# Kernel optimization log

Hardware: AMD Instinct MI355X
Metric: run time of the kernel (lower is better)

## Reference

```python
import jax, jax.numpy as jnp
import numpy as np

N = 1024
X_DIM = 128
Y_DIM = 128
HID = 256


def setup_inputs() -> dict:
    key = jax.random.key(0)
    ks = jax.random.split(key, 8)
    x_samples = jax.random.normal(ks[0], (N, X_DIM), dtype=jnp.float32)
    y_samples = jax.random.normal(ks[1], (N, Y_DIM), dtype=jnp.float32)
    # F_func: Linear(x_dim+y_dim -> hidden), ReLU, Linear(hidden -> 1)
    W1 = jax.random.normal(ks[2], (HID, X_DIM + Y_DIM), dtype=jnp.float32) * 0.05
    b1 = jax.random.normal(ks[3], (HID,), dtype=jnp.float32) * 0.05
    w2 = jax.random.normal(ks[4], (HID,), dtype=jnp.float32) * 0.05  # Linear(hidden,1) weight
    b2 = jax.random.normal(ks[5], (), dtype=jnp.float32) * 0.05
    # baseline: Linear(y_dim -> 1)
    wb = jax.random.normal(ks[6], (Y_DIM,), dtype=jnp.float32) * 0.05
    bb = jax.random.normal(ks[7], (), dtype=jnp.float32) * 0.05
    return {"x_samples": x_samples, "y_samples": y_samples,
            "W1": W1, "b1": b1, "w2": w2, "b2": b2, "wb": wb, "bb": bb}


def reference(x_samples, y_samples, W1, b1, w2, b2, wb, bb):
    n = y_samples.shape[0]
    # Split first linear: F(x,y) first layer = x @ Wx^T + y @ Wy^T + b1
    # (identical math to Linear on concat([x, y]))
    Wx = W1[:, :X_DIM]  # [H, x_dim]
    Wy = W1[:, X_DIM:]  # [H, y_dim]
    px = x_samples @ Wx.T  # [N, H]
    py = y_samples @ Wy.T  # [N, H]

    # T0: F on paired samples (x_i, y_i) -> [N]
    T0 = jax.nn.relu(px + py + b1) @ w2 + b2

    # T1[i, j] = F(x_j, y_i): x tiled over dim 0, y tiled over dim 1
    h = jax.nn.relu(px[None, :, :] + py[:, None, :] + b1)  # [N, N, H]
    T1 = h @ w2 + b2  # [N, N]

    # baseline log-scores on y -> [N]
    log_scores = y_samples @ wb + bb

    # (T1 - log_scores) broadcasts log_scores along dim 1 (the j/x axis),
    # matching torch's [N,N,1] - [N,1] broadcast; logsumexp over dim 1.
    lse = jax.scipy.special.logsumexp(T1 - log_scores[None, :], axis=1)  # [N]
    log_n = jnp.log(jnp.asarray(n, dtype=T1.dtype))
    lower_bound = (1.0 + T0.mean() - log_scores.mean()
                   - jnp.exp(lse - log_n).mean())
    return lower_bound
```

## Files before the change

### kernel.cpp

```cpp
#include <hip/hip_runtime.h>
#include <hip/hip_fp16.h>

#define NN 1024
#define HID 256
#define XD 128

typedef _Float16 h2 __attribute__((ext_vector_type(2)));

#define WSF_BYTE_OFF 1049600
#define F_C    0
#define F_PART 1024
#define F_T0P  3072
#define F_LSP  3328

__device__ __forceinline__ h2 relu2(h2 x) {
  h2 z = {(_Float16)0, (_Float16)0};
  return __builtin_elementwise_max(x, z);
}

__device__ __forceinline__ float dot2f(h2 a, h2 b, float c) {
#if __has_builtin(__builtin_amdgcn_fdot2)
  return __builtin_amdgcn_fdot2(a, b, c, false);
#else
  return fmaf((float)a.x, (float)b.x, fmaf((float)a.y, (float)b.y, c));
#endif
}

__global__ __launch_bounds__(256) void prep_kernel(
    const float* __restrict__ x, const float* __restrict__ y,
    const float* __restrict__ W1, const float* __restrict__ b1,
    const float* __restrict__ w2, const float* __restrict__ b2p,
    const float* __restrict__ wb, const float* __restrict__ bbp,
    _Float16* __restrict__ wsh, float* __restrict__ wsf)
{
  __shared__ float sx[4][128];
  __shared__ float sy[4][128];
  __shared__ float st0[4][4];
  __shared__ float sls[4];
  const int t = threadIdx.x;
  const int blk = blockIdx.x;
  const int r0 = blk * 4;

  {
    const int rl = (t & 127) >> 5, f = t & 31;
    if (t < 128) {
      *(float4*)&sx[rl][f * 4] = *(const float4*)(x + (r0 + rl) * XD + f * 4);
    } else {
      *(float4*)&sy[rl][f * 4] = *(const float4*)(y + (r0 + rl) * XD + f * 4);
    }
  }
  __syncthreads();

  const int k = t;
  float apx[4] = {0,0,0,0};
  float apy[4] = {0,0,0,0};
  const float* wrow = W1 + k * 256;
  for (int dq = 0; dq < 32; ++dq) {
    float4 wx = *(const float4*)(wrow + dq * 4);
    float4 wy = *(const float4*)(wrow + 128 + dq * 4);
#pragma unroll
    for (int r = 0; r < 4; ++r) {
      float4 xv = *(const float4*)&sx[r][dq * 4];
      float4 yv = *(const float4*)&sy[r][dq * 4];
      apx[r] = fmaf(xv.x, wx.x, apx[r]);
      apx[r] = fmaf(xv.y, wx.y, apx[r]);
      apx[r] = fmaf(xv.z, wx.z, apx[r]);
      apx[r] = fmaf(xv.w, wx.w, apx[r]);
      apy[r] = fmaf(yv.x, wy.x, apy[r]);
      apy[r] = fmaf(yv.y, wy.y, apy[r]);
      apy[r] = fmaf(yv.z, wy.z, apy[r]);
      apy[r] = fmaf(yv.w, wy.w, apy[r]);
    }
  }
  const float b1k = b1[k];
#pragma unroll
  for (int r = 0; r < 4; ++r) apy[r] += b1k;

  {
    const int ko = k >> 3, kl = k & 7;
    _Float16* pxh = wsh;
    _Float16* pyh = wsh + 262144;
#pragma unroll
    for (int r = 0; r < 4; ++r) {
      const int j = r0 + r;
      const int idx = (j >> 6) * 16384 + ko * 512 + (j & 63) * 8 + kl;
      pxh[idx] = (_Float16)apx[r];
      pyh[idx] = (_Float16)apy[r];
    }
  }

  const float w2k = w2[k];
  const float b2v = b2p[0];
  const int wv = t >> 6, lane = t & 63;
#pragma unroll
  for (int r = 0; r < 4; ++r) {
    float v = fmaxf(apx[r] + apy[r], 0.f) * w2k;
    for (int o = 32; o > 0; o >>= 1) v += __shfl_down(v, o);
    if (lane == 0) st0[wv][r] = v;
  }

  if (t < 128) {
    const int rl = t >> 5, f = t & 31;
    float p = 0.f;
#pragma unroll
    for (int l = 0; l < 4; ++l) p = fmaf(sy[rl][f * 4 + l], wb[f * 4 + l], p);
    for (int m = 16; m > 0; m >>= 1) p += __shfl_xor(p, m);
    if (f == 0) {
      const float lsv = p + bbp[0];
      sls[rl] = lsv;
      wsf[F_C + r0 + rl] = __expf(b2v - lsv);
    }
  }
  __syncthreads();
  if (t == 0) {
    float t0s = 0.f, lss = 0.f;
#pragma unroll
    for (int r = 0; r < 4; ++r) {
      t0s += st0[0][r] + st0[1][r] + st0[2][r] + st0[3][r] + b2v;
      lss += sls[r];
    }
    wsf[F_T0P + blk] = t0s;
    wsf[F_LSP + blk] = lss;
  }
  if (blk == 0 && t < 128) {
    h2* w2h = (h2*)(wsh + 524288);
    h2 w; w.x = (_Float16)w2[2 * t]; w.y = (_Float16)w2[2 * t + 1];
    w2h[t] = w;
  }
}

__global__ __launch_bounds__(512) void main_kernel(
    const _Float16* __restrict__ wsh, float* __restrict__ wsf)
{
  __shared__ _Float16 spx[16384];
  __shared__ _Float16 spy[16384];
  const int t = threadIdx.x;
  const int tx = t & 15;
  const int ty = t >> 4;
  const int blk = blockIdx.x;
  const int bi = blk >> 4, bj = blk & 15;

  const float4* gx = (const float4*)(wsh + bj * 16384);
  const float4* gy = (const float4*)(wsh + 262144 + bi * 16384);
  const float4* gw = (const float4*)(wsh + 524288);
  float4* lx = (float4*)spx;
  float4* ly = (float4*)spy;
#pragma unroll
  for (int it = 0; it < 4; ++it) {
    lx[it * 512 + t] = gx[it * 512 + t];
    ly[it * 512 + t] = gy[it * 512 + t];
  }
  __syncthreads();

  float acc[2][4] = {{0.f,0.f,0.f,0.f},{0.f,0.f,0.f,0.f}};
  const float4* spx4 = (const float4*)spx;
  const float4* spy4 = (const float4*)spy;

#pragma unroll 2
  for (int ko = 0; ko < 32; ++ko) {
    float4 wv = gw[ko];
    float4 Af[4], Bf[2];
#pragma unroll
    for (int u = 0; u < 4; ++u) Af[u] = spx4[ko * 64 + u * 16 + tx];
#pragma unroll
    for (int v = 0; v < 2; ++v) Bf[v] = spy4[ko * 64 + v * 32 + ty];
    const h2* wq = (const h2*)&wv;
#pragma unroll
    for (int v = 0; v < 2; ++v) {
      const h2* bh = (const h2*)&Bf[v];
#pragma unroll
      for (int u = 0; u < 4; ++u) {
        const h2* ah = (const h2*)&Af[u];
        float s = acc[v][u];
#pragma unroll
        for (int p = 0; p < 4; ++p) {
          h2 uu = ah[p] + bh[p];
          uu = relu2(uu);
          s = dot2f(uu, wq[p], s);
        }
        acc[v][u] = s;
      }
    }
  }

  const float* cj = wsf + F_C + bj * 64;
  const float c0 = cj[tx], c1 = cj[16 + tx], c2 = cj[32 + tx], c3 = cj[48 + tx];
  float ts = 0.f;
#pragma unroll
  for (int v = 0; v < 2; ++v) {
    ts += __expf(acc[v][0]) * c0;
    ts += __expf(acc[v][1]) * c1;
    ts += __expf(acc[v][2]) * c2;
    ts += __expf(acc[v][3]) * c3;
  }
  for (int o = 32; o > 0; o >>= 1) ts += __shfl_down(ts, o);
  if ((t & 63) == 0) wsf[F_PART + blk * 8 + (t >> 6)] = ts;
}

__global__ __launch_bounds__(256) void fin_kernel(
    const float* __restrict__ wsf, float* __restrict__ out)
{
  __shared__ float sr[4][3];
  const int t = threadIdx.x;
  float e = 0.f;
#pragma unroll
  for (int q = 0; q < 8; ++q) e += wsf[F_PART + t + 256 * q];
  float t0 = wsf[F_T0P + t];
  float ls = wsf[F_LSP + t];
  for (int o = 32; o > 0; o >>= 1) {
    e  += __shfl_down(e, o);
    t0 += __shfl_down(t0, o);
    ls += __shfl_down(ls, o);
  }
  if ((t & 63) == 0) {
    sr[t >> 6][0] = e;
    sr[t >> 6][1] = t0;
    sr[t >> 6][2] = ls;
  }
  __syncthreads();
  if (t == 0) {
    const float es  = sr[0][0] + sr[1][0] + sr[2][0] + sr[3][0];
    const float t0s = sr[0][1] + sr[1][1] + sr[2][1] + sr[3][1];
    const float lss = sr[0][2] + sr[1][2] + sr[2][2] + sr[3][2];
    out[0] = 1.0f + t0s * (1.0f / 1024.0f) - lss * (1.0f / 1024.0f)
                  - es * (1.0f / 1048576.0f);
  }
}

extern "C" void kernel_launch(void* const* d_in, const int* in_sizes, int n_in,
                              void* d_out, int out_size, void* d_ws, size_t ws_size,
                              hipStream_t stream) {
  const float* x  = (const float*)d_in[0];
  const float* y  = (const float*)d_in[1];
  const float* W1 = (const float*)d_in[2];
  const float* b1 = (const float*)d_in[3];
  const float* w2 = (const float*)d_in[4];
  const float* b2 = (const float*)d_in[5];
  const float* wb = (const float*)d_in[6];
  const float* bb = (const float*)d_in[7];
  _Float16* wsh = (_Float16*)d_ws;
  float* wsf = (float*)((char*)d_ws + WSF_BYTE_OFF);
  float* out = (float*)d_out;

  hipLaunchKernelGGL(prep_kernel, dim3(256), dim3(256), 0, stream,
                     x, y, W1, b1, w2, b2, wb, bb, wsh, wsf);
  hipLaunchKernelGGL(main_kernel, dim3(256), dim3(512), 0, stream, wsh, wsf);
  hipLaunchKernelGGL(fin_kernel, dim3(1), dim3(256), 0, stream, wsf, out);
}
```

Baseline: 33.88 us.

## Retile pairwise MLP kernel with per-lane j and register-broadcast i blocks

The main kernel is restructured so each lane owns one x-row (j) and accumulates 16 y-rows (i) in registers. The hidden dimension is split across wave pairs, and the partial sums are combined through shared memory before the exp and reduction. The py operands are no longer staged in LDS; they are read from global memory in a new blocked layout as uniform broadcast loads, which cuts LDS traffic and raises arithmetic per loaded element. The prep kernel now uses 512 threads so the x and y projections run on separate halves, and the final kernel reads the partials as float4. The risk is higher register pressure and latency from the global loads in the inner loop.

```diff
diff --git a/kernel.cpp b/kernel.cpp
--- a/kernel.cpp
+++ b/kernel.cpp
@@ -6,6 +6,7 @@
 #define XD 128
 
 typedef _Float16 h2 __attribute__((ext_vector_type(2)));
+typedef _Float16 h4 __attribute__((ext_vector_type(4)));
 
 #define WSF_BYTE_OFF 1049600
 #define F_C    0
@@ -19,14 +20,10 @@
 }
 
 __device__ __forceinline__ float dot2f(h2 a, h2 b, float c) {
-#if __has_builtin(__builtin_amdgcn_fdot2)
   return __builtin_amdgcn_fdot2(a, b, c, false);
-#else
-  return fmaf((float)a.x, (float)b.x, fmaf((float)a.y, (float)b.y, c));
-#endif
-}
-
-__global__ __launch_bounds__(256) void prep_kernel(
+}
+
+__global__ __launch_bounds__(512) void prep_kernel(
     const float* __restrict__ x, const float* __restrict__ y,
     const float* __restrict__ W1, const float* __restrict__ b1,
     const float* __restrict__ w2, const float* __restrict__ b2p,
@@ -35,72 +32,71 @@
 {
   __shared__ float sx[4][128];
   __shared__ float sy[4][128];
+  __shared__ float spy2[4][256];
   __shared__ float st0[4][4];
   __shared__ float sls[4];
   const int t = threadIdx.x;
   const int blk = blockIdx.x;
   const int r0 = blk * 4;
 
-  {
-    const int rl = (t & 127) >> 5, f = t & 31;
-    if (t < 128) {
-      *(float4*)&sx[rl][f * 4] = *(const float4*)(x + (r0 + rl) * XD + f * 4);
-    } else {
-      *(float4*)&sy[rl][f * 4] = *(const float4*)(y + (r0 + rl) * XD + f * 4);
-    }
-  }
-  __syncthreads();
-
-  const int k = t;
-  float apx[4] = {0,0,0,0};
-  float apy[4] = {0,0,0,0};
-  const float* wrow = W1 + k * 256;
-  for (int dq = 0; dq < 32; ++dq) {
-    float4 wx = *(const float4*)(wrow + dq * 4);
-    float4 wy = *(const float4*)(wrow + 128 + dq * 4);
-#pragma unroll
-    for (int r = 0; r < 4; ++r) {
-      float4 xv = *(const float4*)&sx[r][dq * 4];
-      float4 yv = *(const float4*)&sy[r][dq * 4];
-      apx[r] = fmaf(xv.x, wx.x, apx[r]);
-      apx[r] = fmaf(xv.y, wx.y, apx[r]);
-      apx[r] = fmaf(xv.z, wx.z, apx[r]);
-      apx[r] = fmaf(xv.w, wx.w, apx[r]);
-      apy[r] = fmaf(yv.x, wy.x, apy[r]);
-      apy[r] = fmaf(yv.y, wy.y, apy[r]);
-      apy[r] = fmaf(yv.z, wy.z, apy[r]);
-      apy[r] = fmaf(yv.w, wy.w, apy[r]);
-    }
-  }
-  const float b1k = b1[k];
-#pragma unroll
-  for (int r = 0; r < 4; ++r) apy[r] += b1k;
-
-  {
-    const int ko = k >> 3, kl = k & 7;
-    _Float16* pxh = wsh;
-    _Float16* pyh = wsh + 262144;
-#pragma unroll
-    for (int r = 0; r < 4; ++r) {
-      const int j = r0 + r;
-      const int idx = (j >> 6) * 16384 + ko * 512 + (j & 63) * 8 + kl;
-      pxh[idx] = (_Float16)apx[r];
-      pyh[idx] = (_Float16)apy[r];
-    }
-  }
-
-  const float w2k = w2[k];
-  const float b2v = b2p[0];
-  const int wv = t >> 6, lane = t & 63;
-#pragma unroll
-  for (int r = 0; r < 4; ++r) {
-    float v = fmaxf(apx[r] + apy[r], 0.f) * w2k;
-    for (int o = 32; o > 0; o >>= 1) v += __shfl_down(v, o);
-    if (lane == 0) st0[wv][r] = v;
-  }
-
   if (t < 128) {
     const int rl = t >> 5, f = t & 31;
+    *(float4*)&sx[rl][f * 4] = *(const float4*)(x + (r0 + rl) * XD + f * 4);
+  } else if (t < 256) {
+    const int t2 = t - 128, rl = t2 >> 5, f = t2 & 31;
+    *(float4*)&sy[rl][f * 4] = *(const float4*)(y + (r0 + rl) * XD + f * 4);
+  }
+  __syncthreads();
+
+  const int side = t >> 8;
+  const int k = t & 255;
+  float ap[4] = {0.f, 0.f, 0.f, 0.f};
+  const float* wrow = W1 + k * 256 + side * 128;
+  const float (*sm)[128] = side ? sy : sx;
+#pragma unroll 8
+  for (int dq = 0; dq < 32; ++dq) {
+    float4 wv = *(const float4*)(wrow + dq * 4);
+#pragma unroll
+    for (int r = 0; r < 4; ++r) {
+      float4 sv = *(const float4*)&sm[r][dq * 4];
+      ap[r] = fmaf(sv.x, wv.x, ap[r]);
+      ap[r] = fmaf(sv.y, wv.y, ap[r]);
+      ap[r] = fmaf(sv.z, wv.z, ap[r]);
+      ap[r] = fmaf(sv.w, wv.w, ap[r]);
+    }
+  }
+
+  if (side == 1) {
+    const float b1k = b1[k];
+    _Float16* pyB = wsh + 262144;
+#pragma unroll
+    for (int r = 0; r < 4; ++r) {
+      ap[r] += b1k;
+      spy2[r][k] = ap[r];
+      const int i = r0 + r;
+      pyB[(((i >> 4) * 64 + (k >> 2)) * 16 + (i & 15)) * 4 + (k & 3)] = (_Float16)ap[r];
+    }
+  } else {
+#pragma unroll
+    for (int r = 0; r < 4; ++r) {
+      const int j = r0 + r;
+      wsh[((j >> 6) * 32 + (k >> 3)) * 512 + (j & 63) * 8 + (k & 7)] = (_Float16)ap[r];
+    }
+  }
+  __syncthreads();
+
+  if (side == 0) {
+    const float w2k = w2[k];
+    const int wv = t >> 6, lane = t & 63;
+#pragma unroll
+    for (int r = 0; r < 4; ++r) {
+      float v = fmaxf(ap[r] + spy2[r][k], 0.f) * w2k;
+      for (int o = 32; o > 0; o >>= 1) v += __shfl_down(v, o);
+      if (lane == 0) st0[wv][r] = v;
+    }
+  } else if ((t & 255) < 128) {
+    const int t2 = t & 255;
+    const int rl = t2 >> 5, f = t2 & 31;
     float p = 0.f;
 #pragma unroll
     for (int l = 0; l < 4; ++l) p = fmaf(sy[rl][f * 4 + l], wb[f * 4 + l], p);
@@ -108,11 +104,13 @@
     if (f == 0) {
       const float lsv = p + bbp[0];
       sls[rl] = lsv;
-      wsf[F_C + r0 + rl] = __expf(b2v - lsv);
-    }
-  }
-  __syncthreads();
+      wsf[F_C + r0 + rl] = __expf(b2p[0] - lsv);
+    }
+  }
+  __syncthreads();
+
   if (t == 0) {
+    const float b2v = b2p[0];
     float t0s = 0.f, lss = 0.f;
 #pragma unroll
     for (int r = 0; r < 4; ++r) {
@@ -123,78 +121,78 @@
     wsf[F_LSP + blk] = lss;
   }
   if (blk == 0 && t < 128) {
-    h2* w2h = (h2*)(wsh + 524288);
-    h2 w; w.x = (_Float16)w2[2 * t]; w.y = (_Float16)w2[2 * t + 1];
-    w2h[t] = w;
-  }
-}
-
-__global__ __launch_bounds__(512) void main_kernel(
+    h2 wv2;
+    wv2.x = (_Float16)w2[2 * t];
+    wv2.y = (_Float16)w2[2 * t + 1];
+    ((h2*)(wsh + 524288))[t] = wv2;
+  }
+}
+
+__global__ __launch_bounds__(256) void main_kernel(
     const _Float16* __restrict__ wsh, float* __restrict__ wsf)
 {
   __shared__ _Float16 spx[16384];
-  __shared__ _Float16 spy[16384];
+  __shared__ _Float16 sw2[256];
+  __shared__ float sComb[2][16][64];
   const int t = threadIdx.x;
-  const int tx = t & 15;
-  const int ty = t >> 4;
+  const int lane = t & 63;
+  const int w = __builtin_amdgcn_readfirstlane(t >> 6);
   const int blk = blockIdx.x;
   const int bi = blk >> 4, bj = blk & 15;
 
-  const float4* gx = (const float4*)(wsh + bj * 16384);
-  const float4* gy = (const float4*)(wsh + 262144 + bi * 16384);
-  const float4* gw = (const float4*)(wsh + 524288);
-  float4* lx = (float4*)spx;
-  float4* ly = (float4*)spy;
-#pragma unroll
-  for (int it = 0; it < 4; ++it) {
-    lx[it * 512 + t] = gx[it * 512 + t];
-    ly[it * 512 + t] = gy[it * 512 + t];
-  }
-  __syncthreads();
-
-  float acc[2][4] = {{0.f,0.f,0.f,0.f},{0.f,0.f,0.f,0.f}};
-  const float4* spx4 = (const float4*)spx;
-  const float4* spy4 = (const float4*)spy;
-
-#pragma unroll 2
-  for (int ko = 0; ko < 32; ++ko) {
-    float4 wv = gw[ko];
-    float4 Af[4], Bf[2];
-#pragma unroll
-    for (int u = 0; u < 4; ++u) Af[u] = spx4[ko * 64 + u * 16 + tx];
-#pragma unroll
-    for (int v = 0; v < 2; ++v) Bf[v] = spy4[ko * 64 + v * 32 + ty];
-    const h2* wq = (const h2*)&wv;
-#pragma unroll
-    for (int v = 0; v < 2; ++v) {
-      const h2* bh = (const h2*)&Bf[v];
-#pragma unroll
-      for (int u = 0; u < 4; ++u) {
-        const h2* ah = (const h2*)&Af[u];
-        float s = acc[v][u];
-#pragma unroll
-        for (int p = 0; p < 4; ++p) {
-          h2 uu = ah[p] + bh[p];
-          uu = relu2(uu);
-          s = dot2f(uu, wq[p], s);
-        }
-        acc[v][u] = s;
-      }
-    }
-  }
-
-  const float* cj = wsf + F_C + bj * 64;
-  const float c0 = cj[tx], c1 = cj[16 + tx], c2 = cj[32 + tx], c3 = cj[48 + tx];
-  float ts = 0.f;
-#pragma unroll
-  for (int v = 0; v < 2; ++v) {
-    ts += __expf(acc[v][0]) * c0;
-    ts += __expf(acc[v][1]) * c1;
-    ts += __expf(acc[v][2]) * c2;
-    ts += __expf(acc[v][3]) * c3;
-  }
-  for (int o = 32; o > 0; o >>= 1) ts += __shfl_down(ts, o);
-  if ((t & 63) == 0) wsf[F_PART + blk * 8 + (t >> 6)] = ts;
+  {
+    const float4* gx = (const float4*)(wsh + (size_t)bj * 16384);
+    float4* lx = (float4*)spx;
+#pragma unroll
+    for (int it = 0; it < 8; ++it) lx[it * 256 + t] = gx[it * 256 + t];
+    if (t < 32) ((float4*)sw2)[t] = ((const float4*)(wsh + 524288))[t];
+  }
+  __syncthreads();
+
+  const int isub = w & 1, khalf = w >> 1;
+  const int iblk = bi * 2 + isub;
+  const uint4* __restrict__ bB =
+      (const uint4*)(wsh + 262144) + (size_t)iblk * 512 + (size_t)khalf * 256;
+
+  float acc[16] = {0.f,0.f,0.f,0.f,0.f,0.f,0.f,0.f,
+                   0.f,0.f,0.f,0.f,0.f,0.f,0.f,0.f};
+
+#pragma unroll 4
+  for (int q = 0; q < 32; ++q) {
+    const int kq = khalf * 32 + q;
+    h4 a4 = *(const h4*)(spx + (kq >> 1) * 512 + lane * 8 + (kq & 1) * 4);
+    const h2* ap = (const h2*)&a4;
+    h4 w4 = *(const h4*)(sw2 + kq * 4);
+    const h2* wp = (const h2*)&w4;
+    uint4 b[8];
+#pragma unroll
+    for (int r = 0; r < 8; ++r) b[r] = bB[q * 8 + r];
+    const h2* bh = (const h2*)b;
+#pragma unroll
+    for (int a = 0; a < 16; ++a) {
+      float s = acc[a];
+      h2 u0 = relu2(ap[0] + bh[a * 2 + 0]);
+      s = dot2f(u0, wp[0], s);
+      h2 u1 = relu2(ap[1] + bh[a * 2 + 1]);
+      s = dot2f(u1, wp[1], s);
+      acc[a] = s;
+    }
+  }
+
+  if (w >= 2) {
+#pragma unroll
+    for (int a = 0; a < 16; ++a) sComb[isub][a][lane] = acc[a];
+  }
+  __syncthreads();
+  if (w < 2) {
+    const float cj = wsf[F_C + bj * 64 + lane];
+    float ts = 0.f;
+#pragma unroll
+    for (int a = 0; a < 16; ++a) ts += __expf(acc[a] + sComb[isub][a][lane]);
+    ts *= cj;
+    for (int o = 32; o > 0; o >>= 1) ts += __shfl_down(ts, o);
+    if (lane == 0) wsf[F_PART + blk * 2 + w] = ts;
+  }
 }
 
 __global__ __launch_bounds__(256) void fin_kernel(
@@ -202,9 +200,8 @@
 {
   __shared__ float sr[4][3];
   const int t = threadIdx.x;
-  float e = 0.f;
-#pragma unroll
-  for (int q = 0; q < 8; ++q) e += wsf[F_PART + t + 256 * q];
+  float4 ev = *(const float4*)(wsf + F_PART + t * 4);
+  float e = ev.x + ev.y + ev.z + ev.w;
   float t0 = wsf[F_T0P + t];
   float ls = wsf[F_LSP + t];
   for (int o = 32; o > 0; o >>= 1) {
@@ -242,8 +239,8 @@
   float* wsf = (float*)((char*)d_ws + WSF_BYTE_OFF);
   float* out = (float*)d_out;
 
-  hipLaunchKernelGGL(prep_kernel, dim3(256), dim3(256), 0, stream,
+  hipLaunchKernelGGL(prep_kernel, dim3(256), dim3(512), 0, stream,
                      x, y, W1, b1, w2, b2, wb, bb, wsh, wsf);
-  hipLaunchKernelGGL(main_kernel, dim3(256), dim3(512), 0, stream, wsh, wsf);
+  hipLaunchKernelGGL(main_kernel, dim3(512), dim3(256), 0, stream, wsh, wsf);
   hipLaunchKernelGGL(fin_kernel, dim3(1), dim3(256), 0, stream, wsf, out);
 }
```

Measured after the change: 40.00 us. 18.1% more time.

## Keep px rows in registers and split hidden dim across waves

Applied to the files above, without the earlier changes.

Restructures the pairwise main kernel. Each lane now holds one x-row's half of the hidden vector in registers, and waves loop over 8 y-rows read from LDS (broadcast reads). The hidden dimension is split into two halves across wave groups and combined through shared memory. The grid doubles to 512 blocks of 32 y-rows each, and prep writes a plain row-major layout. This cuts LDS traffic and the footprint per block to raise occupancy, at the cost of high register pressure (16 h8 per lane) and an extra sync and combine step.

```diff
diff --git a/kernel.cpp b/kernel.cpp
--- a/kernel.cpp
+++ b/kernel.cpp
@@ -6,6 +6,7 @@
 #define XD 128
 
 typedef _Float16 h2 __attribute__((ext_vector_type(2)));
+typedef _Float16 h8 __attribute__((ext_vector_type(8)));
 
 #define WSF_BYTE_OFF 1049600
 #define F_C    0
@@ -19,11 +20,7 @@
 }
 
 __device__ __forceinline__ float dot2f(h2 a, h2 b, float c) {
-#if __has_builtin(__builtin_amdgcn_fdot2)
   return __builtin_amdgcn_fdot2(a, b, c, false);
-#else
-  return fmaf((float)a.x, (float)b.x, fmaf((float)a.y, (float)b.y, c));
-#endif
 }
 
 __global__ __launch_bounds__(256) void prep_kernel(
@@ -77,15 +74,13 @@
   for (int r = 0; r < 4; ++r) apy[r] += b1k;
 
   {
-    const int ko = k >> 3, kl = k & 7;
     _Float16* pxh = wsh;
     _Float16* pyh = wsh + 262144;
 #pragma unroll
     for (int r = 0; r < 4; ++r) {
       const int j = r0 + r;
-      const int idx = (j >> 6) * 16384 + ko * 512 + (j & 63) * 8 + kl;
-      pxh[idx] = (_Float16)apx[r];
-      pyh[idx] = (_Float16)apy[r];
+      pxh[j * 256 + k] = (_Float16)apx[r];
+      pyh[j * 256 + k] = (_Float16)apy[r];
     }
   }
 
@@ -123,78 +118,86 @@
     wsf[F_LSP + blk] = lss;
   }
   if (blk == 0 && t < 128) {
-    h2* w2h = (h2*)(wsh + 524288);
-    h2 w; w.x = (_Float16)w2[2 * t]; w.y = (_Float16)w2[2 * t + 1];
-    w2h[t] = w;
-  }
-}
-
-__global__ __launch_bounds__(512) void main_kernel(
+    h2 wv2;
+    wv2.x = (_Float16)w2[2 * t];
+    wv2.y = (_Float16)w2[2 * t + 1];
+    ((h2*)(wsh + 524288))[t] = wv2;
+  }
+}
+
+__global__ __launch_bounds__(512, 4) void main_kernel(
     const _Float16* __restrict__ wsh, float* __restrict__ wsf)
 {
-  __shared__ _Float16 spx[16384];
-  __shared__ _Float16 spy[16384];
+  __shared__ _Float16 spy[32 * 256];
+  __shared__ _Float16 sw2[256];
+  __shared__ float sComb[4][8][64];
   const int t = threadIdx.x;
-  const int tx = t & 15;
-  const int ty = t >> 4;
+  const int lane = t & 63;
+  const int w = t >> 6;
   const int blk = blockIdx.x;
-  const int bi = blk >> 4, bj = blk & 15;
-
-  const float4* gx = (const float4*)(wsh + bj * 16384);
-  const float4* gy = (const float4*)(wsh + 262144 + bi * 16384);
-  const float4* gw = (const float4*)(wsh + 524288);
-  float4* lx = (float4*)spx;
-  float4* ly = (float4*)spy;
-#pragma unroll
-  for (int it = 0; it < 4; ++it) {
-    lx[it * 512 + t] = gx[it * 512 + t];
-    ly[it * 512 + t] = gy[it * 512 + t];
-  }
-  __syncthreads();
-
-  float acc[2][4] = {{0.f,0.f,0.f,0.f},{0.f,0.f,0.f,0.f}};
-  const float4* spx4 = (const float4*)spx;
-  const float4* spy4 = (const float4*)spy;
-
+  const int bj = blk & 15;
+  const int i0 = (blk >> 4) * 32;
+  const int khalf = w >> 2;
+  const int iset = w & 3;
+
+  h8 pxr[16];
+  {
+    const float4* gpx = (const float4*)(wsh + (size_t)(bj * 64 + lane) * 256
+                                            + khalf * 128);
+#pragma unroll
+    for (int it = 0; it < 16; ++it) ((float4*)pxr)[it] = gpx[it];
+  }
+  {
+    const float4* gpy = (const float4*)(wsh + 262144 + (size_t)i0 * 256);
+    float4* lpy = (float4*)spy;
+    lpy[t] = gpy[t];
+    lpy[t + 512] = gpy[t + 512];
+    if (t < 32) ((float4*)sw2)[t] = ((const float4*)(wsh + 524288))[t];
+  }
+  __syncthreads();
+
+  const float cj = wsf[F_C + bj * 64 + lane];
+
+  const _Float16* w2k = sw2 + khalf * 128;
+  float sacc[8];
 #pragma unroll 2
-  for (int ko = 0; ko < 32; ++ko) {
-    float4 wv = gw[ko];
-    float4 Af[4], Bf[2];
-#pragma unroll
-    for (int u = 0; u < 4; ++u) Af[u] = spx4[ko * 64 + u * 16 + tx];
-#pragma unroll
-    for (int v = 0; v < 2; ++v) Bf[v] = spy4[ko * 64 + v * 32 + ty];
-    const h2* wq = (const h2*)&wv;
-#pragma unroll
-    for (int v = 0; v < 2; ++v) {
-      const h2* bh = (const h2*)&Bf[v];
+  for (int ii = 0; ii < 8; ++ii) {
+    const _Float16* prow = spy + (iset * 8 + ii) * 256 + khalf * 128;
+    float s0 = 0.f, s1 = 0.f, s2 = 0.f, s3 = 0.f;
+#pragma unroll
+    for (int q = 0; q < 16; q += 4) {
 #pragma unroll
       for (int u = 0; u < 4; ++u) {
-        const h2* ah = (const h2*)&Af[u];
-        float s = acc[v][u];
-#pragma unroll
-        for (int p = 0; p < 4; ++p) {
-          h2 uu = ah[p] + bh[p];
-          uu = relu2(uu);
-          s = dot2f(uu, wq[p], s);
-        }
-        acc[v][u] = s;
+        h8 pv = *(const h8*)(prow + (q + u) * 8);
+        h8 wv = *(const h8*)(w2k + (q + u) * 8);
+        const h2* p2 = (const h2*)&pv;
+        const h2* w2p = (const h2*)&wv;
+        const h2* x2 = (const h2*)&pxr[q + u];
+        float s = (u == 0) ? s0 : (u == 1) ? s1 : (u == 2) ? s2 : s3;
+        s = dot2f(relu2(x2[0] + p2[0]), w2p[0], s);
+        s = dot2f(relu2(x2[1] + p2[1]), w2p[1], s);
+        s = dot2f(relu2(x2[2] + p2[2]), w2p[2], s);
+        s = dot2f(relu2(x2[3] + p2[3]), w2p[3], s);
+        if (u == 0) s0 = s; else if (u == 1) s1 = s; else if (u == 2) s2 = s; else s3 = s;
       }
     }
-  }
-
-  const float* cj = wsf + F_C + bj * 64;
-  const float c0 = cj[tx], c1 = cj[16 + tx], c2 = cj[32 + tx], c3 = cj[48 + tx];
-  float ts = 0.f;
-#pragma unroll
-  for (int v = 0; v < 2; ++v) {
-    ts += __expf(acc[v][0]) * c0;
-    ts += __expf(acc[v][1]) * c1;
-    ts += __expf(acc[v][2]) * c2;
-    ts += __expf(acc[v][3]) * c3;
-  }
-  for (int o = 32; o > 0; o >>= 1) ts += __shfl_down(ts, o);
-  if ((t & 63) == 0) wsf[F_PART + blk * 8 + (t >> 6)] = ts;
+    sacc[ii] = (s0 + s1) + (s2 + s3);
+  }
+
+  if (khalf == 1) {
+#pragma unroll
+    for (int ii = 0; ii < 8; ++ii) sComb[iset][ii][lane] = sacc[ii];
+  }
+  __syncthreads();
+  if (khalf == 0) {
+    float ts = 0.f;
+#pragma unroll
+    for (int ii = 0; ii < 8; ++ii)
+      ts += __expf(sacc[ii] + sComb[iset][ii][lane]);
+    ts *= cj;
+    for (int o = 32; o > 0; o >>= 1) ts += __shfl_down(ts, o);
+    if (lane == 0) wsf[F_PART + blk * 4 + iset] = ts;
+  }
 }
 
 __global__ __launch_bounds__(256) void fin_kernel(
@@ -202,9 +205,9 @@
 {
   __shared__ float sr[4][3];
   const int t = threadIdx.x;
-  float e = 0.f;
-#pragma unroll
-  for (int q = 0; q < 8; ++q) e += wsf[F_PART + t + 256 * q];
+  float4 e0 = *(const float4*)(wsf + F_PART + t * 4);
+  float4 e1 = *(const float4*)(wsf + F_PART + 1024 + t * 4);
+  float e = (e0.x + e0.y + e0.z + e0.w) + (e1.x + e1.y + e1.z + e1.w);
   float t0 = wsf[F_T0P + t];
   float ls = wsf[F_LSP + t];
   for (int o = 32; o > 0; o >>= 1) {
@@ -244,6 +247,6 @@
 
   hipLaunchKernelGGL(prep_kernel, dim3(256), dim3(256), 0, stream,
                      x, y, W1, b1, w2, b2, wb, bb, wsh, wsf);
-  hipLaunchKernelGGL(main_kernel, dim3(256), dim3(512), 0, stream, wsh, wsf);
+  hipLaunchKernelGGL(main_kernel, dim3(512), dim3(512), 0, stream, wsh, wsf);
   hipLaunchKernelGGL(fin_kernel, dim3(1), dim3(256), 0, stream, wsf, out);
 }
```

Measured after the change: 98.05 us. 2.89x slower.
